# Kernel optimization log

Hardware: AMD Instinct MI355X
Metric: run time of the kernel (lower is better)

The kernel has to match this reference:

```python
import jax, jax.numpy as jnp
import numpy as np

NEG_INF = -1e20

# Dims: s=512 samples, b=2048 background, t=32 trees, f=64 features, h=128 hidden, y=1
S, B, T, F, H, Y = 512, 2048, 32, 64, 128, 1


def setup_inputs() -> dict:
    key = jax.random.key(0)
    ks = jax.random.split(key, 8)
    X = jax.random.normal(ks[0], (S, F), dtype=jnp.float32)
    background_X = jax.random.normal(ks[1], (B, F), dtype=jnp.float32)
    background_y = jax.random.normal(ks[2], (B, Y), dtype=jnp.float32)
    neighbors_hot = jax.random.randint(ks[3], (S, B, T), 0, 2).astype(jnp.bool_)
    # encoder params: Linear(F->H), Tanh, Linear(H->H)  (n_layers=2)
    W1 = jax.random.normal(ks[4], (F, H), dtype=jnp.float32) / np.sqrt(F)
    b1 = jnp.zeros((H,), dtype=jnp.float32)
    W2 = jax.random.normal(ks[5], (H, H), dtype=jnp.float32) / np.sqrt(H)
    b2 = jnp.zeros((H,), dtype=jnp.float32)
    return {"X": X, "background_X": background_X, "background_y": background_y,
            "neighbors_hot": neighbors_hot, "W1": W1, "b1": b1, "W2": W2, "b2": b2}


def reference(X, background_X, background_y, neighbors_hot, W1, b1, W2, b2):
    def encode(x):
        return jnp.tanh(x @ W1 + b1) @ W2 + b2  # Linear-Tanh-Linear

    X_enc = encode(X)                    # (s, h)
    bg_enc = encode(background_X)        # (b, h)
    dots = X_enc @ bg_enc.T              # (s, b)
    # broadcast over trees + mask, softmax over background axis
    scores = jnp.where(neighbors_hot, dots[:, :, None], NEG_INF)  # (s, b, t)
    first_alphas = jax.nn.softmax(scores, axis=1)                 # (s, b, t)
    first_leaf_xs = jnp.einsum('sbt,bf->stf', first_alphas, background_X)
    first_leaf_y = jnp.einsum('sbt,by->sty', first_alphas, background_y)
    return first_leaf_xs, first_leaf_y, first_alphas
```

## Files before the change

kernel.cpp:

```cpp
#include <hip/hip_runtime.h>
#include <hip/hip_bf16.h>

#define NS 512
#define NB 2048
#define NT 32
#define NF 64
#define NH 128
#define NFX 80

#define OY  ((size_t)NS * NT * NF)
#define OA  (OY + (size_t)NS * NT)

typedef __attribute__((ext_vector_type(8))) short bf16x8;
typedef __attribute__((ext_vector_type(4))) float f32x4;

__device__ __forceinline__ unsigned short f2bfu(float x) {
    __hip_bfloat16 h = __float2bfloat16(x);
    return __builtin_bit_cast(unsigned short, h);
}

__global__ void detect_layout_k(const unsigned char* m, int* flag) {
    __shared__ int any1;
    if (threadIdx.x == 0) any1 = 0;
    __syncthreads();
    for (int i = threadIdx.x; i < 4096; i += blockDim.x)
        if ((i & 3) != 0 && m[i] != 0) any1 = 1;
    __syncthreads();
    if (threadIdx.x == 0) *flag = any1;
}

__device__ __forceinline__ unsigned int pack16_bytes(uint4 v) {
    unsigned int r = 0;
    unsigned int xs[4] = {v.x, v.y, v.z, v.w};
    #pragma unroll
    for (int i = 0; i < 4; ++i) {
        unsigned int x = xs[i];
        unsigned int t = (x | ((x & 0x7F7F7F7Fu) + 0x7F7F7F7Fu)) & 0x80808080u;
        t >>= 7;
        unsigned int n = (t | (t >> 7) | (t >> 14) | (t >> 21)) & 0xFu;
        r |= n << (i * 4);
    }
    return r;
}

__global__ __launch_bounds__(256) void prep_k(const void* mask, const int* flag,
        unsigned long long* pm,
        const float* __restrict__ X, const float* __restrict__ bgX,
        const float* __restrict__ bgy,
        const float* __restrict__ W1, const float* __restrict__ b1,
        const float* __restrict__ W2, const float* __restrict__ b2,
        float* __restrict__ enc, unsigned short* __restrict__ bgXT2) {
    __shared__ float cbuf[64 * 65];
    const int blk = blockIdx.x;
    const int tid = threadIdx.x;

    if (blk < 2048) {
        const int w = blk * 256 + tid;
        if (*flag) {
            const uint4* mb = (const uint4*)mask;
            uint4 q0 = mb[(size_t)w * 4 + 0];
            uint4 q1 = mb[(size_t)w * 4 + 1];
            uint4 q2 = mb[(size_t)w * 4 + 2];
            uint4 q3 = mb[(size_t)w * 4 + 3];
            unsigned long long r =  (unsigned long long)pack16_bytes(q0)
                                 | ((unsigned long long)pack16_bytes(q1) << 16)
                                 | ((unsigned long long)pack16_bytes(q2) << 32)
                                 | ((unsigned long long)pack16_bytes(q3) << 48);
            pm[w] = r;
        } else {
            const uint4* mi = (const uint4*)mask;
            unsigned long long r = 0;
            #pragma unroll
            for (int i = 0; i < 16; ++i) {
                uint4 v = mi[(size_t)w * 16 + i];
                unsigned int b = (v.x ? 1u : 0u) | (v.y ? 2u : 0u) |
                                 (v.z ? 4u : 0u) | (v.w ? 8u : 0u);
                r |= (unsigned long long)b << (i * 4);
            }
            pm[w] = r;
        }
        return;
    }

    if (blk < 2048 + 320) {
        const int r0 = (blk - 2048) * 8;
        float* xr = cbuf;
        float* hr = cbuf + 512;
        if (tid < 128) {
            int r = tid >> 4, c = (tid & 15) * 4;
            int row = r0 + r;
            const float* src = (row < NS) ? (X + (size_t)row * NF)
                                          : (bgX + (size_t)(row - NS) * NF);
            *(float4*)(&xr[r * 64 + c]) = *(const float4*)(src + c);
        }
        __syncthreads();
        const int j = tid & 127, h = tid >> 7;
        float a1[4] = {b1[j], b1[j], b1[j], b1[j]};
        for (int f = 0; f < NF; ++f) {
            float wv = W1[f * NH + j];
            #pragma unroll
            for (int rr = 0; rr < 4; ++rr) a1[rr] = fmaf(xr[(h * 4 + rr) * 64 + f], wv, a1[rr]);
        }
        #pragma unroll
        for (int rr = 0; rr < 4; ++rr) hr[(h * 4 + rr) * 128 + j] = tanhf(a1[rr]);
        __syncthreads();
        float a2[4] = {b2[j], b2[j], b2[j], b2[j]};
        for (int k = 0; k < NH; ++k) {
            float wv = W2[k * NH + j];
            #pragma unroll
            for (int rr = 0; rr < 4; ++rr) a2[rr] = fmaf(hr[(h * 4 + rr) * 128 + k], wv, a2[rr]);
        }
        #pragma unroll
        for (int rr = 0; rr < 4; ++rr) enc[(size_t)(r0 + h * 4 + rr) * NH + j] = a2[rr];
        return;
    }

    {
        const int b0 = (blk - 2368) * 64;
        float (*t_lds)[65] = (float(*)[65])cbuf;
        #pragma unroll
        for (int it = 0; it < 4; ++it) {
            int idx = (it * 256 + tid) * 4;
            int r = idx >> 6, c = idx & 63;
            *(float4*)(&t_lds[r][c]) = *(const float4*)(bgX + (size_t)(b0 + r) * NF + c);
        }
        __syncthreads();
        const int f = tid >> 2, sg = (tid & 3) * 16;
        union { unsigned short u[16]; uint4 q[2]; } pk;
        #pragma unroll
        for (int i = 0; i < 16; ++i) pk.u[i] = f2bfu(t_lds[sg + i][f]);
        uint4* dst = (uint4*)(bgXT2 + (size_t)f * NB + b0 + sg);
        dst[0] = pk.q[0];
        dst[1] = pk.q[1];
        if (tid < 64) {
            int b = b0 + tid;
            bgXT2[(size_t)64 * NB + b] = f2bfu(bgy[b]);
            bgXT2[(size_t)65 * NB + b] = 0x3F80;
            #pragma unroll
            for (int ff = 66; ff < NFX; ++ff) bgXT2[(size_t)ff * NB + b] = 0;
        }
    }
}

__global__ __launch_bounds__(256) void dots_k(const float* __restrict__ Xe,
        const float* __restrict__ Be, float* __restrict__ dots) {
    __shared__ float At[64 * 68];
    __shared__ float Bt[64 * 68];
    const int s0 = blockIdx.y * 64, b0 = blockIdx.x * 64;
    const int tid = threadIdx.x;
    const int ts = tid & 15, tb = tid >> 4;
    float acc[4][4] = {};
    for (int kt = 0; kt < 2; ++kt) {
        __syncthreads();
        #pragma unroll
        for (int it = 0; it < 4; ++it) {
            int idx = tid * 4 + it * 1024;
            int r = idx >> 6, k = idx & 63;
            *(float4*)(&At[r * 68 + k]) = *(const float4*)(Xe + (size_t)(s0 + r) * NH + kt * 64 + k);
            *(float4*)(&Bt[r * 68 + k]) = *(const float4*)(Be + (size_t)(b0 + r) * NH + kt * 64 + k);
        }
        __syncthreads();
        #pragma unroll 4
        for (int k = 0; k < 64; ++k) {
            float a[4], bv[4];
            #pragma unroll
            for (int i = 0; i < 4; ++i) a[i] = At[(ts + 16 * i) * 68 + k];
            #pragma unroll
            for (int jj = 0; jj < 4; ++jj) bv[jj] = Bt[(tb * 4 + jj) * 68 + k];
            #pragma unroll
            for (int i = 0; i < 4; ++i)
                #pragma unroll
                for (int jj = 0; jj < 4; ++jj)
                    acc[i][jj] = fmaf(a[i], bv[jj], acc[i][jj]);
        }
    }
    #pragma unroll
    for (int i = 0; i < 4; ++i) {
        float4 v = make_float4(acc[i][0], acc[i][1], acc[i][2], acc[i][3]);
        *(float4*)(&dots[(size_t)(s0 + ts + 16 * i) * NB + b0 + tb * 4]) = v;
    }
}

__global__ __launch_bounds__(256) void fusedA_k(float* __restrict__ dots,
        const unsigned long long* __restrict__ pmask,
        const unsigned short* __restrict__ bgXT2,
        float* __restrict__ rden_g, float* __restrict__ out) {
    __shared__ __align__(16) unsigned int mrow[NB];
    __shared__ __align__(16) unsigned short e_bf[NB];
    __shared__ float part[3 * NT * NFX];
    __shared__ float wmax[4];
    __shared__ float rden_l[NT];
    __shared__ float ytmp[NT];

    const int s = blockIdx.x;
    const int tid = threadIdx.x;
    const int lane = tid & 63, w = tid >> 6;
    const int lo = lane & 15, hi = lane >> 4;

    float* drow = dots + (size_t)s * NB;
    float4 d0 = *(const float4*)(drow + tid * 8);
    float4 d1 = *(const float4*)(drow + tid * 8 + 4);
    const uint4* pmrow = (const uint4*)((const unsigned int*)pmask + (size_t)s * NB);
    *(uint4*)(&mrow[tid * 4]) = pmrow[tid];
    *(uint4*)(&mrow[(tid + 256) * 4]) = pmrow[tid + 256];
    float pmax = fmaxf(fmaxf(fmaxf(d0.x, d0.y), fmaxf(d0.z, d0.w)),
                       fmaxf(fmaxf(d1.x, d1.y), fmaxf(d1.z, d1.w)));
    #pragma unroll
    for (int off = 32; off >= 1; off >>= 1)
        pmax = fmaxf(pmax, __shfl_xor(pmax, off, 64));
    if (lane == 0) wmax[w] = pmax;
    __syncthreads();
    const float Ms = fmaxf(fmaxf(wmax[0], wmax[1]), fmaxf(wmax[2], wmax[3]));
    float ev[8] = {d0.x, d0.y, d0.z, d0.w, d1.x, d1.y, d1.z, d1.w};
    union { unsigned short u[8]; uint4 q; } epk;
    #pragma unroll
    for (int q = 0; q < 8; ++q) { ev[q] = __expf(ev[q] - Ms); epk.u[q] = f2bfu(ev[q]); }
    *(float4*)(drow + tid * 8)     = make_float4(ev[0], ev[1], ev[2], ev[3]);
    *(float4*)(drow + tid * 8 + 4) = make_float4(ev[4], ev[5], ev[6], ev[7]);
    *(uint4*)(&e_bf[tid * 8]) = epk.q;
    __syncthreads();

    f32x4 acc[2][5] = {};
    const unsigned short* bptr = bgXT2 + (size_t)lo * NB + w * 512 + hi * 8;
    #pragma unroll 2
    for (int ks = 0; ks < 16; ++ks) {
        const int bb = w * 512 + ks * 32 + hi * 8;
        uint4 ew4 = *(const uint4*)(&e_bf[bb]);
        uint4 m0 = *(const uint4*)(&mrow[bb]);
        uint4 m1 = *(const uint4*)(&mrow[bb + 4]);
        unsigned int ew[4] = {ew4.x, ew4.y, ew4.z, ew4.w};
        unsigned int mv[8] = {m0.x, m0.y, m0.z, m0.w, m1.x, m1.y, m1.z, m1.w};
        unsigned int A0[4], A1[4];
        #pragma unroll
        for (int p = 0; p < 4; ++p) {
            unsigned int mlo = mv[2 * p]     >> lo;
            unsigned int mhi = mv[2 * p + 1] >> lo;
            unsigned int k0 = ((mlo & 1u)       ? 0x0000FFFFu : 0u) |
                              ((mhi & 1u)       ? 0xFFFF0000u : 0u);
            unsigned int k1 = ((mlo & 0x10000u) ? 0x0000FFFFu : 0u) |
                              ((mhi & 0x10000u) ? 0xFFFF0000u : 0u);
            A0[p] = ew[p] & k0;
            A1[p] = ew[p] & k1;
        }
        bf16x8 a0 = __builtin_bit_cast(bf16x8, make_uint4(A0[0], A0[1], A0[2], A0[3]));
        bf16x8 a1 = __builtin_bit_cast(bf16x8, make_uint4(A1[0], A1[1], A1[2], A1[3]));
        #pragma unroll
        for (int n = 0; n < 5; ++n) {
            uint4 bv = *(const uint4*)(bptr + (size_t)n * 16 * NB + ks * 32);
            bf16x8 bfr = __builtin_bit_cast(bf16x8, bv);
            acc[0][n] = __builtin_amdgcn_mfma_f32_16x16x32_bf16(a0, bfr, acc[0][n], 0, 0, 0);
            acc[1][n] = __builtin_amdgcn_mfma_f32_16x16x32_bf16(a1, bfr, acc[1][n], 0, 0, 0);
        }
    }

    if (w > 0) {
        #pragma unroll
        for (int m = 0; m < 2; ++m)
            #pragma unroll
            for (int n = 0; n < 5; ++n)
                #pragma unroll
                for (int r = 0; r < 4; ++r) {
                    int t = m * 16 + hi * 4 + r, f = n * 16 + lo;
                    part[(w - 1) * (NT * NFX) + t * NFX + f] = acc[m][n][r];
                }
    }
    __syncthreads();
    if (w == 0) {
        #pragma unroll
        for (int m = 0; m < 2; ++m)
            #pragma unroll
            for (int r = 0; r < 4; ++r) {
                int t = m * 16 + hi * 4 + r;
                int o = t * NFX + 64 + lo;
                float tot = acc[m][4][r] + part[o] + part[NT * NFX + o] + part[2 * NT * NFX + o];
                if (lo == 0) ytmp[t] = tot;
                if (lo == 1) rden_l[t] = (tot > 0.f) ? 1.f / tot : 0.f;
            }
    }
    __syncthreads();
    if (w == 0) {
        float* xout = out + (size_t)s * NT * NF;
        #pragma unroll
        for (int m = 0; m < 2; ++m)
            #pragma unroll
            for (int n = 0; n < 4; ++n)
                #pragma unroll
                for (int r = 0; r < 4; ++r) {
                    int t = m * 16 + hi * 4 + r, f = n * 16 + lo;
                    int o = t * NFX + f;
                    float tot = acc[m][n][r] + part[o] + part[NT * NFX + o] + part[2 * NT * NFX + o];
                    xout[t * NF + f] = tot * rden_l[t];
                }
    }
    if (tid < 32) {
        out[OY + (size_t)s * NT + tid] = ytmp[tid] * rden_l[tid];
        rden_g[(size_t)s * NT + tid] = rden_l[tid];
    }
}

__global__ __launch_bounds__(256) void alphas_k(const float* __restrict__ e,
        const unsigned int* __restrict__ pmask32, const float* __restrict__ rden_g,
        float* __restrict__ out) {
    const int tid = threadIdx.x;
    const int blk = blockIdx.x;
    const int s = blk >> 3;
    const int tq = tid & 7;
    const f32x4 rd4 = *(const f32x4*)(rden_g + (size_t)s * NT + tq * 4);
    const float* erow = e + (size_t)s * NB;
    const unsigned int* mr = pmask32 + (size_t)s * NB;
    float* aout = out + OA + (size_t)s * NB * NT;
    const int b0 = (blk & 7) * 256 + (tid >> 3);

    float ev[8];
    unsigned int mv[8];
    #pragma unroll
    for (int j = 0; j < 8; ++j) {
        ev[j] = erow[b0 + j * 32];
        mv[j] = mr[b0 + j * 32] >> (tq * 4);
    }
    #pragma unroll
    for (int j = 0; j < 8; ++j) {
        const int b = b0 + j * 32;
        f32x4 v;
        v.x = (mv[j] & 1u) ? ev[j] * rd4.x : 0.f;
        v.y = (mv[j] & 2u) ? ev[j] * rd4.y : 0.f;
        v.z = (mv[j] & 4u) ? ev[j] * rd4.z : 0.f;
        v.w = (mv[j] & 8u) ? ev[j] * rd4.w : 0.f;
        *(f32x4*)(aout + (size_t)b * NT + tq * 4) = v;
    }
}

extern "C" void kernel_launch(void* const* d_in, const int* in_sizes, int n_in,
                              void* d_out, int out_size, void* d_ws, size_t ws_size,
                              hipStream_t stream) {
    (void)in_sizes; (void)n_in; (void)out_size; (void)ws_size;
    const float* X   = (const float*)d_in[0];
    const float* bgX = (const float*)d_in[1];
    const float* bgy = (const float*)d_in[2];
    const void*  nh  = d_in[3];
    const float* W1  = (const float*)d_in[4];
    const float* b1v = (const float*)d_in[5];
    const float* W2  = (const float*)d_in[6];
    const float* b2v = (const float*)d_in[7];
    float* out = (float*)d_out;
    char* ws = (char*)d_ws;

    int* flag = (int*)ws;
    float* enc = (float*)(ws + 4096);
    float* rden_g = (float*)(ws + 4096);
    float* Xe = enc;
    float* Be = enc + (size_t)NS * NH;
    float* dots = (float*)(ws + 4096 + (size_t)(NS + NB) * NH * 4);
    unsigned long long* pmask = (unsigned long long*)((char*)dots + (size_t)NS * NB * 4);
    unsigned short* bgXT2 = (unsigned short*)((char*)pmask + (size_t)NS * NB * NT / 64 * 8);

    detect_layout_k<<<1, 256, 0, stream>>>((const unsigned char*)nh, flag);
    prep_k<<<2048 + 320 + 32, 256, 0, stream>>>(nh, flag, pmask, X, bgX, bgy,
                                                W1, b1v, W2, b2v, enc, bgXT2);
    dots_k<<<dim3(NB / 64, NS / 64), 256, 0, stream>>>(Xe, Be, dots);
    fusedA_k<<<NS, 256, 0, stream>>>(dots, pmask, bgXT2, rden_g, out);
    alphas_k<<<NS * 8, 256, 0, stream>>>(dots, (const unsigned int*)pmask, rden_g, out);
}
```

Before: 112.4 us.

## Fuse dots, softmax-weighted aggregation and alpha writes into one kernel

Removes the separate layout-detect, dots GEMM and alphas kernels. Mask layout detection moves into each prep block. Each per-sample block now computes its row of dot products directly from the encodings with per-thread FMA and a shuffle reduce, then keeps the exponentials in shared memory and writes the alphas itself. This drops the global round trips of the dots/e matrix and two kernel launches. In exchange, every block re-reads all background encodings without tiling, and the cross-wave partial reduction is serialised through a single smaller shared buffer.

After: 144.3 us. 1.28x slower.

```diff
diff --git a/kernel.cpp b/kernel.cpp
--- a/kernel.cpp
+++ b/kernel.cpp
@@ -17,16 +17,6 @@
 __device__ __forceinline__ unsigned short f2bfu(float x) {
     __hip_bfloat16 h = __float2bfloat16(x);
     return __builtin_bit_cast(unsigned short, h);
-}
-
-__global__ void detect_layout_k(const unsigned char* m, int* flag) {
-    __shared__ int any1;
-    if (threadIdx.x == 0) any1 = 0;
-    __syncthreads();
-    for (int i = threadIdx.x; i < 4096; i += blockDim.x)
-        if ((i & 3) != 0 && m[i] != 0) any1 = 1;
-    __syncthreads();
-    if (threadIdx.x == 0) *flag = any1;
 }
 
 __device__ __forceinline__ unsigned int pack16_bytes(uint4 v) {
@@ -43,7 +33,7 @@
     return r;
 }
 
-__global__ __launch_bounds__(256) void prep_k(const void* mask, const int* flag,
+__global__ __launch_bounds__(256) void prep_k(const void* mask,
         unsigned long long* pm,
         const float* __restrict__ X, const float* __restrict__ bgX,
         const float* __restrict__ bgy,
@@ -55,8 +45,18 @@
     const int tid = threadIdx.x;
 
     if (blk < 2048) {
+        int* flagp = (int*)cbuf;
+        if (tid == 0) *flagp = 0;
+        __syncthreads();
+        {
+            uint4 v = ((const uint4*)mask)[tid];
+            if (((v.x | v.y | v.z | v.w) & 0xFFFFFF00u) != 0u) *flagp = 1;
+        }
+        __syncthreads();
+        const int isbyte = *flagp;
+
         const int w = blk * 256 + tid;
-        if (*flag) {
+        if (isbyte) {
             const uint4* mb = (const uint4*)mask;
             uint4 q0 = mb[(size_t)w * 4 + 0];
             uint4 q1 = mb[(size_t)w * 4 + 1];
@@ -142,54 +142,17 @@
     }
 }
 
-__global__ __launch_bounds__(256) void dots_k(const float* __restrict__ Xe,
-        const float* __restrict__ Be, float* __restrict__ dots) {
-    __shared__ float At[64 * 68];
-    __shared__ float Bt[64 * 68];
-    const int s0 = blockIdx.y * 64, b0 = blockIdx.x * 64;
-    const int tid = threadIdx.x;
-    const int ts = tid & 15, tb = tid >> 4;
-    float acc[4][4] = {};
-    for (int kt = 0; kt < 2; ++kt) {
-        __syncthreads();
-        #pragma unroll
-        for (int it = 0; it < 4; ++it) {
-            int idx = tid * 4 + it * 1024;
-            int r = idx >> 6, k = idx & 63;
-            *(float4*)(&At[r * 68 + k]) = *(const float4*)(Xe + (size_t)(s0 + r) * NH + kt * 64 + k);
-            *(float4*)(&Bt[r * 68 + k]) = *(const float4*)(Be + (size_t)(b0 + r) * NH + kt * 64 + k);
-        }
-        __syncthreads();
-        #pragma unroll 4
-        for (int k = 0; k < 64; ++k) {
-            float a[4], bv[4];
-            #pragma unroll
-            for (int i = 0; i < 4; ++i) a[i] = At[(ts + 16 * i) * 68 + k];
-            #pragma unroll
-            for (int jj = 0; jj < 4; ++jj) bv[jj] = Bt[(tb * 4 + jj) * 68 + k];
-            #pragma unroll
-            for (int i = 0; i < 4; ++i)
-                #pragma unroll
-                for (int jj = 0; jj < 4; ++jj)
-                    acc[i][jj] = fmaf(a[i], bv[jj], acc[i][jj]);
-        }
-    }
-    #pragma unroll
-    for (int i = 0; i < 4; ++i) {
-        float4 v = make_float4(acc[i][0], acc[i][1], acc[i][2], acc[i][3]);
-        *(float4*)(&dots[(size_t)(s0 + ts + 16 * i) * NB + b0 + tb * 4]) = v;
-    }
-}
-
-__global__ __launch_bounds__(256) void fusedA_k(float* __restrict__ dots,
-        const unsigned long long* __restrict__ pmask,
+__global__ __launch_bounds__(256, 2) void fused2_k(
+        const float* __restrict__ enc,
+        const unsigned long long* __restrict__ pm,
         const unsigned short* __restrict__ bgXT2,
-        float* __restrict__ rden_g, float* __restrict__ out) {
+        float* __restrict__ out) {
+    __shared__ __align__(16) float e_f32[NB];
     __shared__ __align__(16) unsigned int mrow[NB];
     __shared__ __align__(16) unsigned short e_bf[NB];
-    __shared__ float part[3 * NT * NFX];
+    __shared__ __align__(16) float part[NT * NFX];
     __shared__ float wmax[4];
-    __shared__ float rden_l[NT];
+    __shared__ __align__(16) float rden_l[NT];
     __shared__ float ytmp[NT];
 
     const int s = blockIdx.x;
@@ -197,84 +160,123 @@
     const int lane = tid & 63, w = tid >> 6;
     const int lo = lane & 15, hi = lane >> 4;
 
-    float* drow = dots + (size_t)s * NB;
-    float4 d0 = *(const float4*)(drow + tid * 8);
-    float4 d1 = *(const float4*)(drow + tid * 8 + 4);
-    const uint4* pmrow = (const uint4*)((const unsigned int*)pmask + (size_t)s * NB);
+    const uint4* pmrow = (const uint4*)((const unsigned int*)pm + (size_t)s * NB);
     *(uint4*)(&mrow[tid * 4]) = pmrow[tid];
     *(uint4*)(&mrow[(tid + 256) * 4]) = pmrow[tid + 256];
-    float pmax = fmaxf(fmaxf(fmaxf(d0.x, d0.y), fmaxf(d0.z, d0.w)),
-                       fmaxf(fmaxf(d1.x, d1.y), fmaxf(d1.z, d1.w)));
-    #pragma unroll
-    for (int off = 32; off >= 1; off >>= 1)
-        pmax = fmaxf(pmax, __shfl_xor(pmax, off, 64));
-    if (lane == 0) wmax[w] = pmax;
+
+    {
+        const int kq = tid & 3;
+        const int rg = tid >> 2;
+        f32x4 xq[8];
+        const float* xrow = enc + (size_t)s * NH + kq * 32;
+        #pragma unroll
+        for (int i = 0; i < 8; ++i) xq[i] = *(const f32x4*)(xrow + i * 4);
+        const float* Be = enc + (size_t)NS * NH;
+        float pmax = -3.4e38f;
+        for (int pass = 0; pass < 32; ++pass) {
+            const int b = pass * 64 + rg;
+            const float* brow = Be + (size_t)b * NH + kq * 32;
+            float dp = 0.f;
+            #pragma unroll
+            for (int i = 0; i < 8; ++i) {
+                f32x4 bv = *(const f32x4*)(brow + i * 4);
+                dp += bv.x * xq[i].x + bv.y * xq[i].y + bv.z * xq[i].z + bv.w * xq[i].w;
+            }
+            dp += __shfl_xor(dp, 1, 64);
+            dp += __shfl_xor(dp, 2, 64);
+            if (kq == 0) e_f32[b] = dp;
+            pmax = fmaxf(pmax, dp);
+        }
+        #pragma unroll
+        for (int off = 32; off >= 4; off >>= 1)
+            pmax = fmaxf(pmax, __shfl_xor(pmax, off, 64));
+        if (lane == 0) wmax[w] = pmax;
+    }
     __syncthreads();
-    const float Ms = fmaxf(fmaxf(wmax[0], wmax[1]), fmaxf(wmax[2], wmax[3]));
-    float ev[8] = {d0.x, d0.y, d0.z, d0.w, d1.x, d1.y, d1.z, d1.w};
-    union { unsigned short u[8]; uint4 q; } epk;
-    #pragma unroll
-    for (int q = 0; q < 8; ++q) { ev[q] = __expf(ev[q] - Ms); epk.u[q] = f2bfu(ev[q]); }
-    *(float4*)(drow + tid * 8)     = make_float4(ev[0], ev[1], ev[2], ev[3]);
-    *(float4*)(drow + tid * 8 + 4) = make_float4(ev[4], ev[5], ev[6], ev[7]);
-    *(uint4*)(&e_bf[tid * 8]) = epk.q;
+
+    {
+        const float Ms = fmaxf(fmaxf(wmax[0], wmax[1]), fmaxf(wmax[2], wmax[3]));
+        float4 d0 = *(const float4*)(&e_f32[tid * 8]);
+        float4 d1 = *(const float4*)(&e_f32[tid * 8 + 4]);
+        float ev[8] = {d0.x, d0.y, d0.z, d0.w, d1.x, d1.y, d1.z, d1.w};
+        union { unsigned short u[8]; uint4 q; } epk;
+        #pragma unroll
+        for (int q = 0; q < 8; ++q) { ev[q] = __expf(ev[q] - Ms); epk.u[q] = f2bfu(ev[q]); }
+        *(float4*)(&e_f32[tid * 8])     = make_float4(ev[0], ev[1], ev[2], ev[3]);
+        *(float4*)(&e_f32[tid * 8 + 4]) = make_float4(ev[4], ev[5], ev[6], ev[7]);
+        *(uint4*)(&e_bf[tid * 8]) = epk.q;
+    }
     __syncthreads();
 
     f32x4 acc[2][5] = {};
-    const unsigned short* bptr = bgXT2 + (size_t)lo * NB + w * 512 + hi * 8;
-    #pragma unroll 2
-    for (int ks = 0; ks < 16; ++ks) {
-        const int bb = w * 512 + ks * 32 + hi * 8;
-        uint4 ew4 = *(const uint4*)(&e_bf[bb]);
-        uint4 m0 = *(const uint4*)(&mrow[bb]);
-        uint4 m1 = *(const uint4*)(&mrow[bb + 4]);
-        unsigned int ew[4] = {ew4.x, ew4.y, ew4.z, ew4.w};
-        unsigned int mv[8] = {m0.x, m0.y, m0.z, m0.w, m1.x, m1.y, m1.z, m1.w};
-        unsigned int A0[4], A1[4];
-        #pragma unroll
-        for (int p = 0; p < 4; ++p) {
-            unsigned int mlo = mv[2 * p]     >> lo;
-            unsigned int mhi = mv[2 * p + 1] >> lo;
-            unsigned int k0 = ((mlo & 1u)       ? 0x0000FFFFu : 0u) |
-                              ((mhi & 1u)       ? 0xFFFF0000u : 0u);
-            unsigned int k1 = ((mlo & 0x10000u) ? 0x0000FFFFu : 0u) |
-                              ((mhi & 0x10000u) ? 0xFFFF0000u : 0u);
-            A0[p] = ew[p] & k0;
-            A1[p] = ew[p] & k1;
-        }
-        bf16x8 a0 = __builtin_bit_cast(bf16x8, make_uint4(A0[0], A0[1], A0[2], A0[3]));
-        bf16x8 a1 = __builtin_bit_cast(bf16x8, make_uint4(A1[0], A1[1], A1[2], A1[3]));
-        #pragma unroll
-        for (int n = 0; n < 5; ++n) {
-            uint4 bv = *(const uint4*)(bptr + (size_t)n * 16 * NB + ks * 32);
-            bf16x8 bfr = __builtin_bit_cast(bf16x8, bv);
-            acc[0][n] = __builtin_amdgcn_mfma_f32_16x16x32_bf16(a0, bfr, acc[0][n], 0, 0, 0);
-            acc[1][n] = __builtin_amdgcn_mfma_f32_16x16x32_bf16(a1, bfr, acc[1][n], 0, 0, 0);
-        }
-    }
-
-    if (w > 0) {
-        #pragma unroll
-        for (int m = 0; m < 2; ++m)
-            #pragma unroll
-            for (int n = 0; n < 5; ++n)
+    {
+        const unsigned short* bptr = bgXT2 + (size_t)lo * NB + w * 512 + hi * 8;
+        #pragma unroll 2
+        for (int ks = 0; ks < 16; ++ks) {
+            const int bb = w * 512 + ks * 32 + hi * 8;
+            uint4 ew4 = *(const uint4*)(&e_bf[bb]);
+            uint4 m0 = *(const uint4*)(&mrow[bb]);
+            uint4 m1 = *(const uint4*)(&mrow[bb + 4]);
+            unsigned int ew[4] = {ew4.x, ew4.y, ew4.z, ew4.w};
+            unsigned int mv[8] = {m0.x, m0.y, m0.z, m0.w, m1.x, m1.y, m1.z, m1.w};
+            unsigned int A0[4], A1[4];
+            #pragma unroll
+            for (int p = 0; p < 4; ++p) {
+                unsigned int mlo = mv[2 * p]     >> lo;
+                unsigned int mhi = mv[2 * p + 1] >> lo;
+                unsigned int k0 = ((mlo & 1u)       ? 0x0000FFFFu : 0u) |
+                                  ((mhi & 1u)       ? 0xFFFF0000u : 0u);
+                unsigned int k1 = ((mlo & 0x10000u) ? 0x0000FFFFu : 0u) |
+                                  ((mhi & 0x10000u) ? 0xFFFF0000u : 0u);
+                A0[p] = ew[p] & k0;
+                A1[p] = ew[p] & k1;
+            }
+            bf16x8 a0 = __builtin_bit_cast(bf16x8, make_uint4(A0[0], A0[1], A0[2], A0[3]));
+            bf16x8 a1 = __builtin_bit_cast(bf16x8, make_uint4(A1[0], A1[1], A1[2], A1[3]));
+            #pragma unroll
+            for (int n = 0; n < 5; ++n) {
+                uint4 bv = *(const uint4*)(bptr + (size_t)n * 16 * NB + ks * 32);
+                bf16x8 bfr = __builtin_bit_cast(bf16x8, bv);
+                acc[0][n] = __builtin_amdgcn_mfma_f32_16x16x32_bf16(a0, bfr, acc[0][n], 0, 0, 0);
+                acc[1][n] = __builtin_amdgcn_mfma_f32_16x16x32_bf16(a1, bfr, acc[1][n], 0, 0, 0);
+            }
+        }
+    }
+
+    for (int src = 1; src < 4; ++src) {
+        __syncthreads();
+        if (w == src) {
+            #pragma unroll
+            for (int m = 0; m < 2; ++m)
                 #pragma unroll
-                for (int r = 0; r < 4; ++r) {
-                    int t = m * 16 + hi * 4 + r, f = n * 16 + lo;
-                    part[(w - 1) * (NT * NFX) + t * NFX + f] = acc[m][n][r];
-                }
-    }
-    __syncthreads();
+                for (int n = 0; n < 5; ++n)
+                    #pragma unroll
+                    for (int r = 0; r < 4; ++r) {
+                        int t = m * 16 + hi * 4 + r, f = n * 16 + lo;
+                        part[t * NFX + f] = acc[m][n][r];
+                    }
+        }
+        __syncthreads();
+        if (w == 0) {
+            #pragma unroll
+            for (int m = 0; m < 2; ++m)
+                #pragma unroll
+                for (int n = 0; n < 5; ++n)
+                    #pragma unroll
+                    for (int r = 0; r < 4; ++r) {
+                        int t = m * 16 + hi * 4 + r, f = n * 16 + lo;
+                        acc[m][n][r] += part[t * NFX + f];
+                    }
+        }
+    }
     if (w == 0) {
         #pragma unroll
         for (int m = 0; m < 2; ++m)
             #pragma unroll
             for (int r = 0; r < 4; ++r) {
                 int t = m * 16 + hi * 4 + r;
-                int o = t * NFX + 64 + lo;
-                float tot = acc[m][4][r] + part[o] + part[NT * NFX + o] + part[2 * NT * NFX + o];
-                if (lo == 0) ytmp[t] = tot;
-                if (lo == 1) rden_l[t] = (tot > 0.f) ? 1.f / tot : 0.f;
+                if (lo == 0) ytmp[t] = acc[m][4][r];
+                if (lo == 1) rden_l[t] = (acc[m][4][r] > 0.f) ? 1.f / acc[m][4][r] : 0.f;
             }
     }
     __syncthreads();
@@ -287,46 +289,29 @@
                 #pragma unroll
                 for (int r = 0; r < 4; ++r) {
                     int t = m * 16 + hi * 4 + r, f = n * 16 + lo;
-                    int o = t * NFX + f;
-                    float tot = acc[m][n][r] + part[o] + part[NT * NFX + o] + part[2 * NT * NFX + o];
-                    xout[t * NF + f] = tot * rden_l[t];
+                    xout[t * NF + f] = acc[m][n][r] * rden_l[t];
                 }
     }
     if (tid < 32) {
         out[OY + (size_t)s * NT + tid] = ytmp[tid] * rden_l[tid];
-        rden_g[(size_t)s * NT + tid] = rden_l[tid];
-    }
-}
-
-__global__ __launch_bounds__(256) void alphas_k(const float* __restrict__ e,
-        const unsigned int* __restrict__ pmask32, const float* __restrict__ rden_g,
-        float* __restrict__ out) {
-    const int tid = threadIdx.x;
-    const int blk = blockIdx.x;
-    const int s = blk >> 3;
-    const int tq = tid & 7;
-    const f32x4 rd4 = *(const f32x4*)(rden_g + (size_t)s * NT + tq * 4);
-    const float* erow = e + (size_t)s * NB;
-    const unsigned int* mr = pmask32 + (size_t)s * NB;
-    float* aout = out + OA + (size_t)s * NB * NT;
-    const int b0 = (blk & 7) * 256 + (tid >> 3);
-
-    float ev[8];
-    unsigned int mv[8];
-    #pragma unroll
-    for (int j = 0; j < 8; ++j) {
-        ev[j] = erow[b0 + j * 32];
-        mv[j] = mr[b0 + j * 32] >> (tq * 4);
-    }
-    #pragma unroll
-    for (int j = 0; j < 8; ++j) {
-        const int b = b0 + j * 32;
-        f32x4 v;
-        v.x = (mv[j] & 1u) ? ev[j] * rd4.x : 0.f;
-        v.y = (mv[j] & 2u) ? ev[j] * rd4.y : 0.f;
-        v.z = (mv[j] & 4u) ? ev[j] * rd4.z : 0.f;
-        v.w = (mv[j] & 8u) ? ev[j] * rd4.w : 0.f;
-        *(f32x4*)(aout + (size_t)b * NT + tq * 4) = v;
+    }
+
+    {
+        const int tq = tid & 7;
+        const f32x4 rd4 = *(const f32x4*)(rden_l + tq * 4);
+        float* aout = out + OA + (size_t)s * NB * NT;
+        #pragma unroll 4
+        for (int it = 0; it < 64; ++it) {
+            int b = (tid >> 3) + it * 32;
+            float e = e_f32[b];
+            unsigned int m = mrow[b] >> (tq * 4);
+            f32x4 v;
+            v.x = (m & 1u) ? e * rd4.x : 0.f;
+            v.y = (m & 2u) ? e * rd4.y : 0.f;
+            v.z = (m & 4u) ? e * rd4.z : 0.f;
+            v.w = (m & 8u) ? e * rd4.w : 0.f;
+            *(f32x4*)(aout + (size_t)b * NT + tq * 4) = v;
+        }
     }
 }
 
@@ -345,19 +330,11 @@
     float* out = (float*)d_out;
     char* ws = (char*)d_ws;
 
-    int* flag = (int*)ws;
     float* enc = (float*)(ws + 4096);
-    float* rden_g = (float*)(ws + 4096);
-    float* Xe = enc;
-    float* Be = enc + (size_t)NS * NH;
-    float* dots = (float*)(ws + 4096 + (size_t)(NS + NB) * NH * 4);
-    unsigned long long* pmask = (unsigned long long*)((char*)dots + (size_t)NS * NB * 4);
+    unsigned long long* pmask = (unsigned long long*)((char*)enc + (size_t)(NS + NB) * NH * 4);
     unsigned short* bgXT2 = (unsigned short*)((char*)pmask + (size_t)NS * NB * NT / 64 * 8);
 
-    detect_layout_k<<<1, 256, 0, stream>>>((const unsigned char*)nh, flag);
-    prep_k<<<2048 + 320 + 32, 256, 0, stream>>>(nh, flag, pmask, X, bgX, bgy,
+    prep_k<<<2048 + 320 + 32, 256, 0, stream>>>(nh, pmask, X, bgX, bgy,
                                                 W1, b1v, W2, b2v, enc, bgXT2);
-    dots_k<<<dim3(NB / 64, NS / 64), 256, 0, stream>>>(Xe, Be, dots);
-    fusedA_k<<<NS, 256, 0, stream>>>(dots, pmask, bgXT2, rden_g, out);
-    alphas_k<<<NS * 8, 256, 0, stream>>>(dots, (const unsigned int*)pmask, rden_g, out);
-}
+    fused2_k<<<NS, 256, 0, stream>>>(enc, pmask, bgXT2, out);
+}
```
